# Performance work log

Hardware: AMD Instinct MI355X
Metric: run time of the kernel (lower is better)

The kernel has to match this reference:

```python
import jax, jax.numpy as jnp
import numpy as np

B, BEV = 2, 128
Q = BEV * BEV          # 16384 BEV queries
C, H, L, P = 256, 8, 1, 4
D = C // H             # 32 per-head dim


def setup_inputs() -> dict:
    key = jax.random.key(0)
    ks = jax.random.split(key, 14)
    s = 0.02
    return {
        "query": jax.random.normal(ks[0], (B, Q, C), jnp.float32),
        "value": jax.random.normal(ks[1], (B, Q, C), jnp.float32),
        "identity": jax.random.normal(ks[2], (B, Q, C), jnp.float32),
        "query_pos": jax.random.normal(ks[3], (B, Q, C), jnp.float32),
        "reference_points": jax.random.uniform(ks[4], (B, Q, L, 2), jnp.float32),
        "spatial_shapes": jnp.array([[BEV, BEV]], jnp.int32),
        "level_start_index": jnp.array([0], jnp.int32),
        "Wv": jax.random.normal(ks[5], (C, C), jnp.float32) * s,
        "bv": jnp.zeros((C,), jnp.float32),
        "Woff": jax.random.normal(ks[6], (C, H * L * P * 2), jnp.float32) * s,
        "boff": jax.random.normal(ks[7], (H * L * P * 2,), jnp.float32) * s,
        "Ww": jax.random.normal(ks[8], (C, H * L * P), jnp.float32) * s,
        "bw": jnp.zeros((H * L * P,), jnp.float32),
        "Wo": jax.random.normal(ks[9], (C, C), jnp.float32) * s,
        "bo": jnp.zeros((C,), jnp.float32),
    }


def _deform_attn(q, v, reference_points, shapes_np, Wv, bv, Woff, boff, Ww, bw, Wo, bo):
    b, nq, _ = q.shape
    v = v @ Wv + bv                                             # value_proj
    off = (q @ Woff + boff).reshape(b, nq, H, L, P, 2)          # sampling offsets
    attn = jax.nn.softmax((q @ Ww + bw).reshape(b, nq, H, L * P), axis=-1)
    attn = attn.reshape(b, nq, H, L, P)
    # offset normalizer is (W, H) per level
    norm = jnp.asarray(shapes_np[:, ::-1], jnp.float32)         # [L, 2]
    loc = reference_points[:, :, None, :, None, :] + off / norm[None, None, None, :, None, :]

    out = jnp.zeros((b, H, nq, D), jnp.float32)
    start = 0
    for l in range(L):
        Hl, Wl = int(shapes_np[l, 0]), int(shapes_np[l, 1])
        N = Hl * Wl
        vl = v[:, start:start + N].reshape(b, N, H, D).transpose(0, 2, 1, 3)  # [b,H,N,D]
        start += N
        ll = loc[:, :, :, l]                                    # [b,nq,H,P,2] in [0,1]
        # grid_sample(align_corners=False): pixel coord = loc*size - 0.5
        x = ll[..., 0] * Wl - 0.5
        y = ll[..., 1] * Hl - 0.5
        x0 = jnp.floor(x); y0 = jnp.floor(y)
        dx = x - x0; dy = y - y0
        x0i = x0.astype(jnp.int32); y0i = y0.astype(jnp.int32)

        def gather(ix, iy):
            valid = (ix >= 0) & (ix < Wl) & (iy >= 0) & (iy < Hl)  # zero padding
            idx = jnp.clip(iy, 0, Hl - 1) * Wl + jnp.clip(ix, 0, Wl - 1)
            idx = idx.transpose(0, 2, 1, 3).reshape(b, H, nq * P)
            g = jnp.take_along_axis(vl, idx[..., None], axis=2)   # [b,H,nq*P,D]
            return g * valid.transpose(0, 2, 1, 3).reshape(b, H, nq * P, 1)

        def cw(w):  # corner weight -> [b,H,nq*P,1]
            return w.transpose(0, 2, 1, 3).reshape(b, H, nq * P, 1)

        samp = (gather(x0i, y0i) * cw((1 - dx) * (1 - dy))
                + gather(x0i + 1, y0i) * cw(dx * (1 - dy))
                + gather(x0i, y0i + 1) * cw((1 - dx) * dy)
                + gather(x0i + 1, y0i + 1) * cw(dx * dy))
        samp = samp.reshape(b, H, nq, P, D)
        aw = attn[:, :, :, l].transpose(0, 2, 1, 3)             # [b,H,nq,P]
        out = out + jnp.einsum('bhqpd,bhqp->bhqd', samp, aw)

    out = out.transpose(0, 2, 1, 3).reshape(b, nq, C)
    return out @ Wo + bo                                        # output_proj


def reference(query, value, identity, query_pos, reference_points, spatial_shapes,
              level_start_index, Wv, bv, Woff, boff, Ww, bw, Wo, bo):
    shapes_np = np.asarray(spatial_shapes)                      # static level shapes
    q = query + query_pos
    out = _deform_attn(q, value, reference_points, shapes_np,
                       Wv, bv, Woff, boff, Ww, bw, Wo, bo)
    return out + identity
```

## Files before the change

kernel.cpp:

```cpp
#include <hip/hip_runtime.h>
#include <hip/hip_bf16.h>
#include <stdint.h>

#define Q_TOT 32768
#define CC 256
#define GRID_W 128
#define GRID_H 128

typedef __attribute__((ext_vector_type(8))) short short8;
typedef __attribute__((ext_vector_type(4))) float floatx4;

__device__ __forceinline__ ushort f2bf(float f) {
    union { float f; uint32_t u; } v; v.f = f;
    uint32_t r = (v.u + 0x7fffu + ((v.u >> 16) & 1u)) >> 16;
    return (ushort)r;
}
__device__ __forceinline__ void bf2x2(uint32_t u, float& lo, float& hi) {
    union { uint32_t u; float f; } a, b;
    a.u = u << 16; b.u = u & 0xffff0000u;
    lo = a.f; hi = b.f;
}
__device__ __forceinline__ void async_load16(const void* g, void* l) {
    __builtin_amdgcn_global_load_lds(
        reinterpret_cast<const __attribute__((address_space(1))) uint32_t*>(
            reinterpret_cast<uintptr_t>(g)),
        reinterpret_cast<__attribute__((address_space(3))) uint32_t*>(
            reinterpret_cast<uintptr_t>(l)),
        16, 0, 0);
}

__global__ __launch_bounds__(256)
void prep_weights(const float* __restrict__ Wv, const float* __restrict__ Wo,
                  const float* __restrict__ Woff, const float* __restrict__ Ww,
                  ushort* __restrict__ WvT, ushort* __restrict__ WoT,
                  ushort* __restrict__ WowT)
{
    int idx = blockIdx.x * blockDim.x + threadIdx.x;
    if (idx < 65536) {
        int n = idx >> 8, k = idx & 255;
        WvT[idx] = f2bf(Wv[k * 256 + n]);
    } else if (idx < 131072) {
        int t = idx - 65536; int n = t >> 8, k = t & 255;
        WoT[t] = f2bf(Wo[k * 256 + n]);
    } else if (idx < 155648) {
        int t = idx - 131072; int n = t >> 8, k = t & 255;
        float v = (n < 64) ? Woff[k * 64 + n] : Ww[k * 32 + (n - 64)];
        WowT[t] = f2bf(v);
    }
}

template <int BM, int BN, int WAVE_M, int WAVE_N, bool OUT_BF16, int CONV>
__global__ __launch_bounds__(256)
void gemm_bf16(const void* __restrict__ Av, const float* __restrict__ A2,
               const ushort* __restrict__ Bt,
               const float* __restrict__ bias, const float* __restrict__ res,
               void* __restrict__ Cout, int M, int N, int K)
{
    constexpr int TM = BM / WAVE_M / 16;
    constexpr int TN = BN / WAVE_N / 16;
    __shared__ __align__(16) ushort As[2][BM * 32];
    __shared__ __align__(16) ushort Bs[2][BN * 32];

    const int tid = threadIdx.x;
    const int lane = tid & 63;
    const int wave = tid >> 6;
    const int wm = wave / WAVE_N;
    const int wn = wave % WAVE_N;
    const int quad = lane >> 4;
    const int m16 = lane & 15;
    const int lrow = lane >> 2;
    const int lkk = (lane & 3) * 8;

    const int nwg = gridDim.x * gridDim.y;
    const int hw = blockIdx.y * gridDim.x + blockIdx.x;
    const int t = (hw & 7) * (nwg >> 3) + (hw >> 3);
    const int bx = t % gridDim.x;
    const int by = t / gridDim.x;

    const int row0 = by * BM;
    const int col0 = bx * BN;

    floatx4 acc[TM][TN] = {};

    auto stage = [&](int buf, int k0) {
        #pragma unroll
        for (int i = wave; i < BM / 16; i += 4) {
            const int r = row0 + i * 16 + lrow;
            if constexpr (CONV == 0) {
                const ushort* src = (const ushort*)Av + (size_t)r * K + (k0 + lkk);
                async_load16(src, &As[buf][i * 16 * 32]);
            } else {
                const float* src = (const float*)Av + (size_t)r * K + (k0 + lkk);
                float4 a0 = ((const float4*)src)[0];
                float4 a1 = ((const float4*)src)[1];
                if constexpr (CONV == 2) {
                    const float* s2 = A2 + (size_t)r * K + (k0 + lkk);
                    float4 b0 = ((const float4*)s2)[0];
                    float4 b1 = ((const float4*)s2)[1];
                    a0.x += b0.x; a0.y += b0.y; a0.z += b0.z; a0.w += b0.w;
                    a1.x += b1.x; a1.y += b1.y; a1.z += b1.z; a1.w += b1.w;
                }
                uint4 o;
                o.x = ((uint32_t)f2bf(a0.y) << 16) | f2bf(a0.x);
                o.y = ((uint32_t)f2bf(a0.w) << 16) | f2bf(a0.z);
                o.z = ((uint32_t)f2bf(a1.y) << 16) | f2bf(a1.x);
                o.w = ((uint32_t)f2bf(a1.w) << 16) | f2bf(a1.z);
                *(uint4*)&As[buf][i * 16 * 32 + lrow * 32 + lkk] = o;
            }
        }
        #pragma unroll
        for (int i = wave; i < BN / 16; i += 4) {
            const ushort* src = Bt + (size_t)(col0 + i * 16 + lrow) * K + (k0 + lkk);
            async_load16(src, &Bs[buf][i * 16 * 32]);
        }
    };

    stage(0, 0);
    __syncthreads();

    int cur = 0;
    for (int k0 = 0; k0 < K; k0 += 32) {
        if (k0 + 32 < K) stage(cur ^ 1, k0 + 32);

        short8 af[TM], bfr[TN];
        #pragma unroll
        for (int i = 0; i < TM; ++i)
            af[i] = *(const short8*)&As[cur][(wm * TM * 16 + i * 16 + m16) * 32 + quad * 8];
        #pragma unroll
        for (int j = 0; j < TN; ++j)
            bfr[j] = *(const short8*)&Bs[cur][(wn * TN * 16 + j * 16 + m16) * 32 + quad * 8];
        #pragma unroll
        for (int i = 0; i < TM; ++i)
            #pragma unroll
            for (int j = 0; j < TN; ++j)
                acc[i][j] = __builtin_amdgcn_mfma_f32_16x16x32_bf16(
                    af[i], bfr[j], acc[i][j], 0, 0, 0);

        __syncthreads();
        cur ^= 1;
    }

    #pragma unroll
    for (int i = 0; i < TM; ++i) {
        #pragma unroll
        for (int j = 0; j < TN; ++j) {
            const int gcol = col0 + wn * TN * 16 + j * 16 + m16;
            const float bb = bias[gcol];
            #pragma unroll
            for (int r = 0; r < 4; ++r) {
                const int grow = row0 + wm * TM * 16 + i * 16 + quad * 4 + r;
                float v = acc[i][j][r] + bb;
                if (res) v += res[(size_t)grow * N + gcol];
                if constexpr (OUT_BF16)
                    ((ushort*)Cout)[(size_t)grow * N + gcol] = f2bf(v);
                else
                    ((float*)Cout)[(size_t)grow * N + gcol] = v;
            }
        }
    }
}

#define FBM 64
__global__ __launch_bounds__(256)
void fused_attn(const float* __restrict__ query, const float* __restrict__ qpos,
                const ushort* __restrict__ WowT,
                const float* __restrict__ boff, const float* __restrict__ bw,
                const ushort* __restrict__ v2,
                const float* __restrict__ ref,
                const ushort* __restrict__ WoT,
                const float* __restrict__ bo, const float* __restrict__ identity,
                float* __restrict__ out)
{
    __shared__ __align__(16) char smem[71680];
    ushort* As   = (ushort*)smem;
    ushort* Bsow = (ushort*)(smem + 4096);
    float*  owl  = (float*)(smem + 10240);
    ushort* samp = (ushort*)(smem + 36864);
    ushort* Bwo  = (ushort*)smem;

    const int tid = threadIdx.x;
    const int lane = tid & 63;
    const int wave = tid >> 6;
    const int quad = lane >> 4;
    const int m16 = lane & 15;
    const int lrow = lane >> 2;
    const int lkk = (lane & 3) * 8;
    const int wm = wave >> 1;
    const int wn = wave & 1;

    const int q0 = blockIdx.x * FBM;

    floatx4 aow[2][3] = {};
    for (int k0 = 0; k0 < 256; k0 += 32) {
        {
            const int r = wave * 16 + lrow;
            const float* s1 = query + (size_t)(q0 + r) * 256 + (k0 + lkk);
            const float* s2 = qpos  + (size_t)(q0 + r) * 256 + (k0 + lkk);
            float4 a0 = ((const float4*)s1)[0];
            float4 a1 = ((const float4*)s1)[1];
            float4 b0 = ((const float4*)s2)[0];
            float4 b1 = ((const float4*)s2)[1];
            a0.x += b0.x; a0.y += b0.y; a0.z += b0.z; a0.w += b0.w;
            a1.x += b1.x; a1.y += b1.y; a1.z += b1.z; a1.w += b1.w;
            uint4 o;
            o.x = ((uint32_t)f2bf(a0.y) << 16) | f2bf(a0.x);
            o.y = ((uint32_t)f2bf(a0.w) << 16) | f2bf(a0.z);
            o.z = ((uint32_t)f2bf(a1.y) << 16) | f2bf(a1.x);
            o.w = ((uint32_t)f2bf(a1.w) << 16) | f2bf(a1.z);
            *(uint4*)&As[r * 32 + lkk] = o;
        }
        for (int i = wave; i < 6; i += 4) {
            const ushort* src = WowT + (size_t)(i * 16 + lrow) * 256 + (k0 + lkk);
            async_load16(src, &Bsow[i * 16 * 32]);
        }
        __syncthreads();

        short8 af[2], bfw[3];
        #pragma unroll
        for (int i = 0; i < 2; ++i)
            af[i] = *(const short8*)&As[(wm * 32 + i * 16 + m16) * 32 + quad * 8];
        #pragma unroll
        for (int j = 0; j < 3; ++j)
            bfw[j] = *(const short8*)&Bsow[(wn * 48 + j * 16 + m16) * 32 + quad * 8];
        #pragma unroll
        for (int i = 0; i < 2; ++i)
            #pragma unroll
            for (int j = 0; j < 3; ++j)
                aow[i][j] = __builtin_amdgcn_mfma_f32_16x16x32_bf16(
                    af[i], bfw[j], aow[i][j], 0, 0, 0);
        __syncthreads();
    }
    #pragma unroll
    for (int i = 0; i < 2; ++i)
        #pragma unroll
        for (int j = 0; j < 3; ++j) {
            const int col = wn * 48 + j * 16 + m16;
            const float bb = (col < 64) ? boff[col] : bw[col - 64];
            #pragma unroll
            for (int r = 0; r < 4; ++r)
                owl[(wm * 32 + i * 16 + quad * 4 + r) * 104 + col] = aow[i][j][r] + bb;
        }
    __syncthreads();

    {
        const int ql = tid >> 2;
        const int dg = tid & 3;
        const int qg = q0 + ql;
        const int bb2 = qg >> 14;
        const float rx = ref[(size_t)qg * 2 + 0] * (float)GRID_W;
        const float ry = ref[(size_t)qg * 2 + 1] * (float)GRID_H;
        const ushort* vbase = v2 + (size_t)bb2 * 16384 * 256 + dg * 8;
        const float* owr = &owl[ql * 104];

        #pragma unroll 1
        for (int h = 0; h < 8; ++h) {
            const float w0 = owr[64 + h * 4 + 0], w1 = owr[64 + h * 4 + 1];
            const float w2 = owr[64 + h * 4 + 2], w3 = owr[64 + h * 4 + 3];
            const float mx = fmaxf(fmaxf(w0, w1), fmaxf(w2, w3));
            const float e0 = __expf(w0 - mx), e1 = __expf(w1 - mx);
            const float e2 = __expf(w2 - mx), e3 = __expf(w3 - mx);
            const float inv = 1.f / (e0 + e1 + e2 + e3);
            const float aw[4] = {e0 * inv, e1 * inv, e2 * inv, e3 * inv};

            const ushort* vh = vbase + h * 32;
            float acc8[8] = {};
            #pragma unroll
            for (int p = 0; p < 4; ++p) {
                const float x = rx + owr[h * 8 + p * 2 + 0] - 0.5f;
                const float y = ry + owr[h * 8 + p * 2 + 1] - 0.5f;
                const float x0f = floorf(x), y0f = floorf(y);
                const float dx = x - x0f, dy = y - y0f;
                const int x0 = (int)x0f, y0 = (int)y0f;
                const int x1 = x0 + 1, y1 = y0 + 1;
                const float vx0 = (x0 >= 0 && x0 < GRID_W) ? 1.f : 0.f;
                const float vx1 = (x1 >= 0 && x1 < GRID_W) ? 1.f : 0.f;
                const float vy0 = (y0 >= 0 && y0 < GRID_H) ? 1.f : 0.f;
                const float vy1 = (y1 >= 0 && y1 < GRID_H) ? 1.f : 0.f;
                const int xc0 = min(max(x0, 0), GRID_W - 1);
                const int xc1 = min(max(x1, 0), GRID_W - 1);
                const int yc0 = min(max(y0, 0), GRID_H - 1);
                const int yc1 = min(max(y1, 0), GRID_H - 1);
                const float cw00 = aw[p] * (1.f - dx) * (1.f - dy) * vx0 * vy0;
                const float cw10 = aw[p] * dx * (1.f - dy) * vx1 * vy0;
                const float cw01 = aw[p] * (1.f - dx) * dy * vx0 * vy1;
                const float cw11 = aw[p] * dx * dy * vx1 * vy1;
                const int base0 = yc0 * GRID_W, base1 = yc1 * GRID_W;
                const uint4 r00 = *(const uint4*)(vh + (size_t)(base0 + xc0) * 256);
                const uint4 r10 = *(const uint4*)(vh + (size_t)(base0 + xc1) * 256);
                const uint4 r01 = *(const uint4*)(vh + (size_t)(base1 + xc0) * 256);
                const uint4 r11 = *(const uint4*)(vh + (size_t)(base1 + xc1) * 256);
                float lo, hi;
                bf2x2(r00.x, lo, hi); acc8[0] += cw00 * lo; acc8[1] += cw00 * hi;
                bf2x2(r00.y, lo, hi); acc8[2] += cw00 * lo; acc8[3] += cw00 * hi;
                bf2x2(r00.z, lo, hi); acc8[4] += cw00 * lo; acc8[5] += cw00 * hi;
                bf2x2(r00.w, lo, hi); acc8[6] += cw00 * lo; acc8[7] += cw00 * hi;
                bf2x2(r10.x, lo, hi); acc8[0] += cw10 * lo; acc8[1] += cw10 * hi;
                bf2x2(r10.y, lo, hi); acc8[2] += cw10 * lo; acc8[3] += cw10 * hi;
                bf2x2(r10.z, lo, hi); acc8[4] += cw10 * lo; acc8[5] += cw10 * hi;
                bf2x2(r10.w, lo, hi); acc8[6] += cw10 * lo; acc8[7] += cw10 * hi;
                bf2x2(r01.x, lo, hi); acc8[0] += cw01 * lo; acc8[1] += cw01 * hi;
                bf2x2(r01.y, lo, hi); acc8[2] += cw01 * lo; acc8[3] += cw01 * hi;
                bf2x2(r01.z, lo, hi); acc8[4] += cw01 * lo; acc8[5] += cw01 * hi;
                bf2x2(r01.w, lo, hi); acc8[6] += cw01 * lo; acc8[7] += cw01 * hi;
                bf2x2(r11.x, lo, hi); acc8[0] += cw11 * lo; acc8[1] += cw11 * hi;
                bf2x2(r11.y, lo, hi); acc8[2] += cw11 * lo; acc8[3] += cw11 * hi;
                bf2x2(r11.z, lo, hi); acc8[4] += cw11 * lo; acc8[5] += cw11 * hi;
                bf2x2(r11.w, lo, hi); acc8[6] += cw11 * lo; acc8[7] += cw11 * hi;
            }
            uint4 o;
            o.x = ((uint32_t)f2bf(acc8[1]) << 16) | f2bf(acc8[0]);
            o.y = ((uint32_t)f2bf(acc8[3]) << 16) | f2bf(acc8[2]);
            o.z = ((uint32_t)f2bf(acc8[5]) << 16) | f2bf(acc8[4]);
            o.w = ((uint32_t)f2bf(acc8[7]) << 16) | f2bf(acc8[6]);
            *(uint4*)&samp[ql * 272 + h * 32 + dg * 8] = o;
        }
    }
    __syncthreads();

    auto stageW = [&](int buf, int ks) {
        for (int i = wave; i < 16; i += 4) {
            const ushort* src = WoT + (size_t)(i * 16 + lrow) * 256 + ks * 32 + lkk;
            async_load16(src, &Bwo[buf * 8192 + i * 16 * 32]);
        }
    };
    stageW(0, 0);
    __syncthreads();

    floatx4 acc[2][8] = {};
    int cur = 0;
    for (int ks = 0; ks < 8; ++ks) {
        if (ks + 1 < 8) stageW(cur ^ 1, ks + 1);

        short8 af[2], bfr[8];
        #pragma unroll
        for (int i = 0; i < 2; ++i)
            af[i] = *(const short8*)&samp[(wm * 32 + i * 16 + m16) * 272 + ks * 32 + quad * 8];
        #pragma unroll
        for (int j = 0; j < 8; ++j)
            bfr[j] = *(const short8*)&Bwo[cur * 8192 + (wn * 128 + j * 16 + m16) * 32 + quad * 8];
        #pragma unroll
        for (int i = 0; i < 2; ++i)
            #pragma unroll
            for (int j = 0; j < 8; ++j)
                acc[i][j] = __builtin_amdgcn_mfma_f32_16x16x32_bf16(
                    af[i], bfr[j], acc[i][j], 0, 0, 0);

        __syncthreads();
        cur ^= 1;
    }

    #pragma unroll
    for (int i = 0; i < 2; ++i)
        #pragma unroll
        for (int j = 0; j < 8; ++j) {
            const int gcol = wn * 128 + j * 16 + m16;
            const float bb = bo[gcol];
            #pragma unroll
            for (int r = 0; r < 4; ++r) {
                const int grow = q0 + wm * 32 + i * 16 + quad * 4 + r;
                out[(size_t)grow * 256 + gcol] =
                    acc[i][j][r] + bb + identity[(size_t)grow * 256 + gcol];
            }
        }
}

extern "C" void kernel_launch(void* const* d_in, const int* in_sizes, int n_in,
                              void* d_out, int out_size, void* d_ws, size_t ws_size,
                              hipStream_t stream) {
    const float* query     = (const float*)d_in[0];
    const float* value     = (const float*)d_in[1];
    const float* identity  = (const float*)d_in[2];
    const float* query_pos = (const float*)d_in[3];
    const float* refpts    = (const float*)d_in[4];
    const float* Wv   = (const float*)d_in[7];
    const float* bv   = (const float*)d_in[8];
    const float* Woff = (const float*)d_in[9];
    const float* boff = (const float*)d_in[10];
    const float* Ww   = (const float*)d_in[11];
    const float* bw   = (const float*)d_in[12];
    const float* Wo   = (const float*)d_in[13];
    const float* bo   = (const float*)d_in[14];
    float* out = (float*)d_out;

    char* ws = (char*)d_ws;
    ushort* v2_bf = (ushort*)(ws);
    ushort* WvT   = (ushort*)(ws + 16777216);
    ushort* WoT   = (ushort*)(ws + 16908288);
    ushort* WowT  = (ushort*)(ws + 17039360);

    prep_weights<<<608, 256, 0, stream>>>(Wv, Wo, Woff, Ww, WvT, WoT, WowT);
    gemm_bf16<128, 64, 2, 2, true, 1><<<dim3(4, 256), 256, 0, stream>>>(
        value, nullptr, WvT, bv, nullptr, v2_bf, Q_TOT, 256, 256);
    fused_attn<<<dim3(Q_TOT / FBM), 256, 0, stream>>>(
        query, query_pos, WowT, boff, bw, v2_bf, refpts, WoT, bo, identity, out);
}
```

Baseline: 230.5 us.

## Shrink fused attention tile to 32 queries, load GEMM operands directly from global

Halves the per-block query tile from 64 to 32 rows and drops LDS staging for the offset/weight projection and output projection weights. MFMA operands now come straight from global or L2. The offset/weight tile is kept in bf16 in LDS, and the sampling loop is split so that 8 threads per query each handle 4 heads. These changes cut LDS use from about 70KB to 24KB and set a launch bound of 4 blocks per CU, aiming for higher occupancy to hide the gather latency. In exchange, weights are re-read from cache per wave, and storing offsets in bf16 loses some precision in the sampling locations.

After: 243.7 us. 5.7% more time.

```diff
diff --git a/kernel.cpp b/kernel.cpp
--- a/kernel.cpp
+++ b/kernel.cpp
@@ -160,8 +160,8 @@
     }
 }
 
-#define FBM 64
-__global__ __launch_bounds__(256)
+#define FBM 32
+__global__ __launch_bounds__(256, 4)
 void fused_attn(const float* __restrict__ query, const float* __restrict__ qpos,
                 const ushort* __restrict__ WowT,
                 const float* __restrict__ boff, const float* __restrict__ bw,
@@ -171,103 +171,89 @@
                 const float* __restrict__ bo, const float* __restrict__ identity,
                 float* __restrict__ out)
 {
-    __shared__ __align__(16) char smem[71680];
-    ushort* As   = (ushort*)smem;
-    ushort* Bsow = (ushort*)(smem + 4096);
-    float*  owl  = (float*)(smem + 10240);
-    ushort* samp = (ushort*)(smem + 36864);
-    ushort* Bwo  = (ushort*)smem;
-
-    const int tid = threadIdx.x;
+    __shared__ __align__(16) char smem[24576];
+    ushort* samp = (ushort*)smem;
+    ushort* owl  = (ushort*)(smem + 17408);
+
+    const int tid  = threadIdx.x;
     const int lane = tid & 63;
     const int wave = tid >> 6;
     const int quad = lane >> 4;
-    const int m16 = lane & 15;
-    const int lrow = lane >> 2;
-    const int lkk = (lane & 3) * 8;
+    const int m16  = lane & 15;
     const int wm = wave >> 1;
     const int wn = wave & 1;
-
     const int q0 = blockIdx.x * FBM;
 
-    floatx4 aow[2][3] = {};
+    floatx4 aow[3] = {};
+    #pragma unroll 2
     for (int k0 = 0; k0 < 256; k0 += 32) {
-        {
-            const int r = wave * 16 + lrow;
-            const float* s1 = query + (size_t)(q0 + r) * 256 + (k0 + lkk);
-            const float* s2 = qpos  + (size_t)(q0 + r) * 256 + (k0 + lkk);
-            float4 a0 = ((const float4*)s1)[0];
-            float4 a1 = ((const float4*)s1)[1];
-            float4 b0 = ((const float4*)s2)[0];
-            float4 b1 = ((const float4*)s2)[1];
-            a0.x += b0.x; a0.y += b0.y; a0.z += b0.z; a0.w += b0.w;
-            a1.x += b1.x; a1.y += b1.y; a1.z += b1.z; a1.w += b1.w;
-            uint4 o;
-            o.x = ((uint32_t)f2bf(a0.y) << 16) | f2bf(a0.x);
-            o.y = ((uint32_t)f2bf(a0.w) << 16) | f2bf(a0.z);
-            o.z = ((uint32_t)f2bf(a1.y) << 16) | f2bf(a1.x);
-            o.w = ((uint32_t)f2bf(a1.w) << 16) | f2bf(a1.z);
-            *(uint4*)&As[r * 32 + lkk] = o;
-        }
-        for (int i = wave; i < 6; i += 4) {
-            const ushort* src = WowT + (size_t)(i * 16 + lrow) * 256 + (k0 + lkk);
-            async_load16(src, &Bsow[i * 16 * 32]);
-        }
-        __syncthreads();
-
-        short8 af[2], bfw[3];
-        #pragma unroll
-        for (int i = 0; i < 2; ++i)
-            af[i] = *(const short8*)&As[(wm * 32 + i * 16 + m16) * 32 + quad * 8];
+        const size_t abase = (size_t)(q0 + wm * 16 + m16) * 256 + k0 + quad * 8;
+        float4 a0 = ((const float4*)(query + abase))[0];
+        float4 a1 = ((const float4*)(query + abase))[1];
+        float4 b0 = ((const float4*)(qpos + abase))[0];
+        float4 b1 = ((const float4*)(qpos + abase))[1];
+        a0.x += b0.x; a0.y += b0.y; a0.z += b0.z; a0.w += b0.w;
+        a1.x += b1.x; a1.y += b1.y; a1.z += b1.z; a1.w += b1.w;
+        union { short8 s; uint32_t u[4]; } ua;
+        ua.u[0] = ((uint32_t)f2bf(a0.y) << 16) | f2bf(a0.x);
+        ua.u[1] = ((uint32_t)f2bf(a0.w) << 16) | f2bf(a0.z);
+        ua.u[2] = ((uint32_t)f2bf(a1.y) << 16) | f2bf(a1.x);
+        ua.u[3] = ((uint32_t)f2bf(a1.w) << 16) | f2bf(a1.z);
+        short8 bfw[3];
         #pragma unroll
         for (int j = 0; j < 3; ++j)
-            bfw[j] = *(const short8*)&Bsow[(wn * 48 + j * 16 + m16) * 32 + quad * 8];
-        #pragma unroll
-        for (int i = 0; i < 2; ++i)
-            #pragma unroll
-            for (int j = 0; j < 3; ++j)
-                aow[i][j] = __builtin_amdgcn_mfma_f32_16x16x32_bf16(
-                    af[i], bfw[j], aow[i][j], 0, 0, 0);
-        __syncthreads();
+            bfw[j] = *(const short8*)(WowT +
+                (size_t)(wn * 48 + j * 16 + m16) * 256 + k0 + quad * 8);
+        #pragma unroll
+        for (int j = 0; j < 3; ++j)
+            aow[j] = __builtin_amdgcn_mfma_f32_16x16x32_bf16(
+                ua.s, bfw[j], aow[j], 0, 0, 0);
     }
     #pragma unroll
-    for (int i = 0; i < 2; ++i)
-        #pragma unroll
-        for (int j = 0; j < 3; ++j) {
-            const int col = wn * 48 + j * 16 + m16;
-            const float bb = (col < 64) ? boff[col] : bw[col - 64];
-            #pragma unroll
-            for (int r = 0; r < 4; ++r)
-                owl[(wm * 32 + i * 16 + quad * 4 + r) * 104 + col] = aow[i][j][r] + bb;
-        }
+    for (int j = 0; j < 3; ++j) {
+        const int col = wn * 48 + j * 16 + m16;
+        const float bb = (col < 64) ? boff[col] : bw[col - 64];
+        #pragma unroll
+        for (int r = 0; r < 4; ++r)
+            owl[(wm * 16 + quad * 4 + r) * 100 + col] = f2bf(aow[j][r] + bb);
+    }
     __syncthreads();
 
     {
-        const int ql = tid >> 2;
+        const int ql = tid >> 3;
+        const int hh = (tid >> 2) & 1;
         const int dg = tid & 3;
         const int qg = q0 + ql;
         const int bb2 = qg >> 14;
         const float rx = ref[(size_t)qg * 2 + 0] * (float)GRID_W;
         const float ry = ref[(size_t)qg * 2 + 1] * (float)GRID_H;
         const ushort* vbase = v2 + (size_t)bb2 * 16384 * 256 + dg * 8;
-        const float* owr = &owl[ql * 104];
-
-        #pragma unroll 1
-        for (int h = 0; h < 8; ++h) {
-            const float w0 = owr[64 + h * 4 + 0], w1 = owr[64 + h * 4 + 1];
-            const float w2 = owr[64 + h * 4 + 2], w3 = owr[64 + h * 4 + 3];
+        const uint32_t* owr = (const uint32_t*)&owl[ql * 100];
+
+        #pragma unroll 2
+        for (int hi = 0; hi < 4; ++hi) {
+            const int h = hh * 4 + hi;
+            float w0, w1, w2, w3;
+            bf2x2(owr[32 + h * 2 + 0], w0, w1);
+            bf2x2(owr[32 + h * 2 + 1], w2, w3);
             const float mx = fmaxf(fmaxf(w0, w1), fmaxf(w2, w3));
             const float e0 = __expf(w0 - mx), e1 = __expf(w1 - mx);
             const float e2 = __expf(w2 - mx), e3 = __expf(w3 - mx);
             const float inv = 1.f / (e0 + e1 + e2 + e3);
             const float aw[4] = {e0 * inv, e1 * inv, e2 * inv, e3 * inv};
 
+            float offs[8];
+            bf2x2(owr[h * 4 + 0], offs[0], offs[1]);
+            bf2x2(owr[h * 4 + 1], offs[2], offs[3]);
+            bf2x2(owr[h * 4 + 2], offs[4], offs[5]);
+            bf2x2(owr[h * 4 + 3], offs[6], offs[7]);
+
             const ushort* vh = vbase + h * 32;
             float acc8[8] = {};
             #pragma unroll
             for (int p = 0; p < 4; ++p) {
-                const float x = rx + owr[h * 8 + p * 2 + 0] - 0.5f;
-                const float y = ry + owr[h * 8 + p * 2 + 1] - 0.5f;
+                const float x = rx + offs[p * 2 + 0] - 0.5f;
+                const float y = ry + offs[p * 2 + 1] - 0.5f;
                 const float x0f = floorf(x), y0f = floorf(y);
                 const float dx = x - x0f, dy = y - y0f;
                 const int x0 = (int)x0f, y0 = (int)y0f;
@@ -289,23 +275,23 @@
                 const uint4 r10 = *(const uint4*)(vh + (size_t)(base0 + xc1) * 256);
                 const uint4 r01 = *(const uint4*)(vh + (size_t)(base1 + xc0) * 256);
                 const uint4 r11 = *(const uint4*)(vh + (size_t)(base1 + xc1) * 256);
-                float lo, hi;
-                bf2x2(r00.x, lo, hi); acc8[0] += cw00 * lo; acc8[1] += cw00 * hi;
-                bf2x2(r00.y, lo, hi); acc8[2] += cw00 * lo; acc8[3] += cw00 * hi;
-                bf2x2(r00.z, lo, hi); acc8[4] += cw00 * lo; acc8[5] += cw00 * hi;
-                bf2x2(r00.w, lo, hi); acc8[6] += cw00 * lo; acc8[7] += cw00 * hi;
-                bf2x2(r10.x, lo, hi); acc8[0] += cw10 * lo; acc8[1] += cw10 * hi;
-                bf2x2(r10.y, lo, hi); acc8[2] += cw10 * lo; acc8[3] += cw10 * hi;
-                bf2x2(r10.z, lo, hi); acc8[4] += cw10 * lo; acc8[5] += cw10 * hi;
-                bf2x2(r10.w, lo, hi); acc8[6] += cw10 * lo; acc8[7] += cw10 * hi;
-                bf2x2(r01.x, lo, hi); acc8[0] += cw01 * lo; acc8[1] += cw01 * hi;
-                bf2x2(r01.y, lo, hi); acc8[2] += cw01 * lo; acc8[3] += cw01 * hi;
-                bf2x2(r01.z, lo, hi); acc8[4] += cw01 * lo; acc8[5] += cw01 * hi;
-                bf2x2(r01.w, lo, hi); acc8[6] += cw01 * lo; acc8[7] += cw01 * hi;
-                bf2x2(r11.x, lo, hi); acc8[0] += cw11 * lo; acc8[1] += cw11 * hi;
-                bf2x2(r11.y, lo, hi); acc8[2] += cw11 * lo; acc8[3] += cw11 * hi;
-                bf2x2(r11.z, lo, hi); acc8[4] += cw11 * lo; acc8[5] += cw11 * hi;
-                bf2x2(r11.w, lo, hi); acc8[6] += cw11 * lo; acc8[7] += cw11 * hi;
+                float lo, hi2;
+                bf2x2(r00.x, lo, hi2); acc8[0] += cw00 * lo; acc8[1] += cw00 * hi2;
+                bf2x2(r00.y, lo, hi2); acc8[2] += cw00 * lo; acc8[3] += cw00 * hi2;
+                bf2x2(r00.z, lo, hi2); acc8[4] += cw00 * lo; acc8[5] += cw00 * hi2;
+                bf2x2(r00.w, lo, hi2); acc8[6] += cw00 * lo; acc8[7] += cw00 * hi2;
+                bf2x2(r10.x, lo, hi2); acc8[0] += cw10 * lo; acc8[1] += cw10 * hi2;
+                bf2x2(r10.y, lo, hi2); acc8[2] += cw10 * lo; acc8[3] += cw10 * hi2;
+                bf2x2(r10.z, lo, hi2); acc8[4] += cw10 * lo; acc8[5] += cw10 * hi2;
+                bf2x2(r10.w, lo, hi2); acc8[6] += cw10 * lo; acc8[7] += cw10 * hi2;
+                bf2x2(r01.x, lo, hi2); acc8[0] += cw01 * lo; acc8[1] += cw01 * hi2;
+                bf2x2(r01.y, lo, hi2); acc8[2] += cw01 * lo; acc8[3] += cw01 * hi2;
+                bf2x2(r01.z, lo, hi2); acc8[4] += cw01 * lo; acc8[5] += cw01 * hi2;
+                bf2x2(r01.w, lo, hi2); acc8[6] += cw01 * lo; acc8[7] += cw01 * hi2;
+                bf2x2(r11.x, lo, hi2); acc8[0] += cw11 * lo; acc8[1] += cw11 * hi2;
+                bf2x2(r11.y, lo, hi2); acc8[2] += cw11 * lo; acc8[3] += cw11 * hi2;
+                bf2x2(r11.z, lo, hi2); acc8[4] += cw11 * lo; acc8[5] += cw11 * hi2;
+                bf2x2(r11.w, lo, hi2); acc8[6] += cw11 * lo; acc8[7] += cw11 * hi2;
             }
             uint4 o;
             o.x = ((uint32_t)f2bf(acc8[1]) << 16) | f2bf(acc8[0]);
@@ -317,47 +303,34 @@
     }
     __syncthreads();
 
-    auto stageW = [&](int buf, int ks) {
-        for (int i = wave; i < 16; i += 4) {
-            const ushort* src = WoT + (size_t)(i * 16 + lrow) * 256 + ks * 32 + lkk;
-            async_load16(src, &Bwo[buf * 8192 + i * 16 * 32]);
-        }
-    };
-    stageW(0, 0);
-    __syncthreads();
-
-    floatx4 acc[2][8] = {};
-    int cur = 0;
+    floatx4 acc[2][4] = {};
+    #pragma unroll 2
     for (int ks = 0; ks < 8; ++ks) {
-        if (ks + 1 < 8) stageW(cur ^ 1, ks + 1);
-
-        short8 af[2], bfr[8];
+        short8 af2[2], bfr[4];
         #pragma unroll
         for (int i = 0; i < 2; ++i)
-            af[i] = *(const short8*)&samp[(wm * 32 + i * 16 + m16) * 272 + ks * 32 + quad * 8];
-        #pragma unroll
-        for (int j = 0; j < 8; ++j)
-            bfr[j] = *(const short8*)&Bwo[cur * 8192 + (wn * 128 + j * 16 + m16) * 32 + quad * 8];
+            af2[i] = *(const short8*)&samp[(i * 16 + m16) * 272 + ks * 32 + quad * 8];
+        #pragma unroll
+        for (int j = 0; j < 4; ++j)
+            bfr[j] = *(const short8*)(WoT +
+                (size_t)(wave * 64 + j * 16 + m16) * 256 + ks * 32 + quad * 8);
         #pragma unroll
         for (int i = 0; i < 2; ++i)
             #pragma unroll
-            for (int j = 0; j < 8; ++j)
+            for (int j = 0; j < 4; ++j)
                 acc[i][j] = __builtin_amdgcn_mfma_f32_16x16x32_bf16(
-                    af[i], bfr[j], acc[i][j], 0, 0, 0);
-
-        __syncthreads();
-        cur ^= 1;
+                    af2[i], bfr[j], acc[i][j], 0, 0, 0);
     }
 
     #pragma unroll
     for (int i = 0; i < 2; ++i)
         #pragma unroll
-        for (int j = 0; j < 8; ++j) {
-            const int gcol = wn * 128 + j * 16 + m16;
+        for (int j = 0; j < 4; ++j) {
+            const int gcol = wave * 64 + j * 16 + m16;
             const float bb = bo[gcol];
             #pragma unroll
             for (int r = 0; r < 4; ++r) {
-                const int grow = q0 + wm * 32 + i * 16 + quad * 4 + r;
+                const int grow = q0 + i * 16 + quad * 4 + r;
                 out[(size_t)grow * 256 + gcol] =
                     acc[i][j][r] + bb + identity[(size_t)grow * 256 + gcol];
             }
```
